# Performance work log

Hardware: AMD Instinct MI355X
Metric: run time of the kernel (lower is better)

Reference implementation:

```python
import jax, jax.numpy as jnp
import numpy as np

N = 100000
D = 128
NEG_SLOPE = 0.2


def setup_inputs() -> dict:
    key = jax.random.key(0)
    ks = jax.random.split(key, 10)
    x = jax.random.normal(ks[0], (N, D), dtype=jnp.float32)
    edge_index = jax.random.randint(ks[1], (2, 625000), 0, N, dtype=jnp.int64)
    s = 1.0 / np.sqrt(D)
    W1 = jax.random.uniform(ks[2], (D, D), jnp.float32, -s, s)
    a_src1 = jax.random.uniform(ks[3], (D,), jnp.float32, -s, s)
    a_dst1 = jax.random.uniform(ks[4], (D,), jnp.float32, -s, s)
    b1 = jnp.zeros((D,), jnp.float32)
    W2 = jax.random.uniform(ks[5], (D, D), jnp.float32, -s, s)
    a_src2 = jax.random.uniform(ks[6], (D,), jnp.float32, -s, s)
    a_dst2 = jax.random.uniform(ks[7], (D,), jnp.float32, -s, s)
    b2 = jnp.zeros((D,), jnp.float32)
    return {"x": x, "edge_index": edge_index, "W1": W1, "a_src1": a_src1,
            "a_dst1": a_dst1, "b1": b1, "W2": W2, "a_src2": a_src2,
            "a_dst2": a_dst2, "b2": b2}


def _add_self_loops(edge_index, n):
    loops = jnp.arange(n, dtype=edge_index.dtype)
    return jnp.concatenate([edge_index, jnp.stack([loops, loops])], axis=1)


def _gat_conv(x, src, dst, W, a_src, a_dst, b, n):
    # Linear transform: [N, D]
    h = x @ W
    # Per-node attention logits, gathered onto edges (heads=1)
    e = jnp.take(h @ a_src, src) + jnp.take(h @ a_dst, dst)  # [E]
    e = jax.nn.leaky_relu(e, NEG_SLOPE)
    # Scatter-softmax over destination-node segments (every node has a self loop)
    m = jax.ops.segment_max(e, dst, num_segments=n)
    w = jnp.exp(e - jnp.take(m, dst))
    z = jax.ops.segment_sum(w, dst, num_segments=n)
    alpha = w / jnp.take(z, dst)  # [E]
    # Weighted scatter-add aggregate
    msg = alpha[:, None] * jnp.take(h, src, axis=0)  # [E, D]
    out = jax.ops.segment_sum(msg, dst, num_segments=n)
    return out + b


def reference(x, edge_index, W1, a_src1, a_dst1, b1, W2, a_src2, a_dst2, b2):
    n = x.shape[0]
    ei = _add_self_loops(edge_index, n)
    src, dst = ei[0], ei[1]
    h = jax.nn.relu(_gat_conv(x, src, dst, W1, a_src1, a_dst1, b1, n))
    h = jax.nn.relu(_gat_conv(h, src, dst, W2, a_src2, a_dst2, b2, n))
    return h
```

## Files before the change

### kernel.cpp

```cpp
#include <hip/hip_runtime.h>

#define D 128
#define WS (D + 8)
#define NEG_SLOPE 0.2f
#define SLOTS 20
#define OVF_CAP 4096

using v8f16 = __attribute__((ext_vector_type(8))) _Float16;
using v2h   = __attribute__((ext_vector_type(2))) _Float16;
using f32x4 = __attribute__((ext_vector_type(4))) float;


__global__ __launch_bounds__(256) void prep_kernel(const float* __restrict__ W1,
        const float* __restrict__ W2, _Float16* __restrict__ Wt1,
        _Float16* __restrict__ Wt2, int* __restrict__ cnt,
        int* __restrict__ ovf_n, int n) {
    int t = blockIdx.x * 256 + threadIdx.x;
    if (t == 0) *ovf_n = 0;
    for (int i = t; i < n; i += 32768) cnt[i] = 0;
    int which = t >> 14;
    int idx = t & 16383;
    int k = idx & (D - 1);
    int c = idx >> 7;
    const float* W = which ? W2 : W1;
    _Float16* Wt = which ? Wt2 : Wt1;
    Wt[(size_t)c * D + k] = (_Float16)W[(size_t)k * D + c];
}


template<bool F16IN>
__device__ __forceinline__ void gemm_body(int bid, const void* __restrict__ Xv,
        const _Float16* __restrict__ Wt, const float* __restrict__ a_src,
        const float* __restrict__ a_dst, _Float16* __restrict__ H,
        float* __restrict__ hs, float* __restrict__ hd, int n,
        _Float16* wl) {
    const int lane = threadIdx.x & 63;
    const int wave = threadIdx.x >> 6;
    const int gl = lane & 15;
    const int q = lane >> 4;
    const int row0 = bid * 128 + wave * 16;

    int arow = row0 + gl;
    if (arow >= n) arow = n - 1;

    v8f16 afr[4];
    #pragma unroll
    for (int kc = 0; kc < 4; ++kc) {
        if constexpr (F16IN) {
            const _Float16* Xh = (const _Float16*)Xv;
            afr[kc] = *(const v8f16*)&Xh[(size_t)arow * D + kc * 32 + q * 8];
        } else {
            const float* p = &((const float*)Xv)[(size_t)arow * D + kc * 32 + q * 8];
            float4 x0 = *(const float4*)p;
            float4 x1 = *(const float4*)(p + 4);
            v8f16 t;
            t[0] = (_Float16)x0.x; t[1] = (_Float16)x0.y;
            t[2] = (_Float16)x0.z; t[3] = (_Float16)x0.w;
            t[4] = (_Float16)x1.x; t[5] = (_Float16)x1.y;
            t[6] = (_Float16)x1.z; t[7] = (_Float16)x1.w;
            afr[kc] = t;
        }
    }

    for (int i = threadIdx.x; i < D * D / 8; i += 512) {
        int r = i >> 4;
        int c = (i & 15) * 8;
        *(v8f16*)&wl[r * WS + c] = *(const v8f16*)&Wt[r * D + c];
    }
    __syncthreads();

    f32x4 acc[8];
    #pragma unroll
    for (int t = 0; t < 8; ++t) acc[t] = (f32x4){0.f, 0.f, 0.f, 0.f};

    #pragma unroll
    for (int kc = 0; kc < 4; ++kc) {
        #pragma unroll
        for (int t = 0; t < 8; ++t) {
            v8f16 bfr = *(const v8f16*)&wl[(t * 16 + gl) * WS + kc * 32 + q * 8];
            acc[t] = __builtin_amdgcn_mfma_f32_16x16x32_f16(afr[kc], bfr, acc[t], 0, 0, 0);
        }
    }

    float asv[8], adv[8];
    #pragma unroll
    for (int t = 0; t < 8; ++t) { asv[t] = a_src[t * 16 + gl]; adv[t] = a_dst[t * 16 + gl]; }

    #pragma unroll
    for (int r = 0; r < 4; ++r) {
        int row = row0 + q * 4 + r;
        bool ok = row < n;
        float ps = 0.f, pd = 0.f;
        #pragma unroll
        for (int t = 0; t < 8; ++t) {
            float v = acc[t][r];
            ps = fmaf(v, asv[t], ps);
            pd = fmaf(v, adv[t], pd);
            if (ok) H[(size_t)row * D + t * 16 + gl] = (_Float16)v;
        }
        #pragma unroll
        for (int dlt = 8; dlt > 0; dlt >>= 1) {
            ps += __shfl_down(ps, dlt, 16);
            pd += __shfl_down(pd, dlt, 16);
        }
        if (ok && gl == 0) { hs[row] = ps; hd[row] = pd; }
    }
}


__global__ __launch_bounds__(512) void mega1_kernel(
        const float* __restrict__ x, const _Float16* __restrict__ Wt1,
        const float* __restrict__ a_src1, const float* __restrict__ a_dst1,
        _Float16* __restrict__ h, float* __restrict__ hs, float* __restrict__ hd,
        const int* __restrict__ ei, int* __restrict__ cnt, int* __restrict__ csr,
        int* __restrict__ ovf_n, int* __restrict__ ovf,
        int gb, int e_in, int n) {
    __shared__ _Float16 wl[D * WS];
    int b = blockIdx.x;
    int rid;
    if (b < 2 * gb) {
        if ((b & 1) == 0) {
            gemm_body<false>(b >> 1, x, Wt1, a_src1, a_dst1, h, hs, hd, n, wl);
            return;
        }
        rid = b >> 1;
    } else {
        rid = b - gb;
    }
    int e = rid * 512 + threadIdx.x;
    int tot = e_in + n;
    if (e >= tot) return;
    int s, d;
    if (e < e_in) { s = ei[e]; d = ei[e_in + e]; }
    else          { s = e - e_in; d = s; }
    int r = atomicAdd(&cnt[d], 1);
    if (r < SLOTS) {
        csr[d * SLOTS + r] = s;
    } else {
        int ix = atomicAdd(ovf_n, 1);
        if (ix < OVF_CAP) { ovf[2 * ix] = d; ovf[2 * ix + 1] = s; }
    }
}

__global__ __launch_bounds__(512) void gemm2_kernel(
        const _Float16* __restrict__ tb, const _Float16* __restrict__ Wt2,
        const float* __restrict__ a_src2, const float* __restrict__ a_dst2,
        _Float16* __restrict__ h, float* __restrict__ hs, float* __restrict__ hd,
        int n) {
    __shared__ _Float16 wl[D * WS];
    gemm_body<true>(blockIdx.x, tb, Wt2, a_src2, a_dst2, h, hs, hd, n, wl);
}


__device__ __forceinline__ v2h pack_lo(uint a, uint b) {
    v2h r;
    r.x = __builtin_bit_cast(_Float16, (unsigned short)(a & 0xffffu));
    r.y = __builtin_bit_cast(_Float16, (unsigned short)(b & 0xffffu));
    return r;
}
__device__ __forceinline__ v2h pack_hi(uint a, uint b) {
    v2h r;
    r.x = __builtin_bit_cast(_Float16, (unsigned short)(a >> 16));
    r.y = __builtin_bit_cast(_Float16, (unsigned short)(b >> 16));
    return r;
}
__device__ __forceinline__ float lo_f(uint a) {
    return (float)__builtin_bit_cast(_Float16, (unsigned short)(a & 0xffffu));
}
__device__ __forceinline__ float hi_f(uint a) {
    return (float)__builtin_bit_cast(_Float16, (unsigned short)(a >> 16));
}

template<bool OUT_F16>
__global__ __launch_bounds__(256) void aggregate_kernel(
        const _Float16* __restrict__ h, const float* __restrict__ hs,
        const float* __restrict__ hd, const int* __restrict__ cnt,
        const int* __restrict__ csr, const int* __restrict__ ovf_n,
        const int* __restrict__ ovf, const float* __restrict__ bias,
        float* __restrict__ outf, _Float16* __restrict__ outb, int n) {
    int node = blockIdx.x * 4 + (threadIdx.x >> 6);
    if (node >= n) return;
    int lane = threadIdx.x & 63;
    int grp = lane >> 4;
    int gl = lane & 15;
    int deg = cnt[node];
    int mind = deg < SLOTS ? deg : SLOTS;
    const int base = node * SLOTS;
    float hdn = hd[node];
    const uint* hp = (const uint*)h;

    float acc[8] = {0.f, 0.f, 0.f, 0.f, 0.f, 0.f, 0.f, 0.f};
    float z = 0.f;

    int nt = (mind + 7) >> 3;

    for (int u = 0; u < nt; ++u) {
        int i0 = u * 8 + grp * 2;
        bool a0 = i0 < mind;
        bool a1 = i0 + 1 < mind;
        int s0 = a0 ? csr[base + i0] : node;
        int s1 = a1 ? csr[base + i0 + 1] : node;
        uint4 rA = *(const uint4*)(hp + ((size_t)s0 << 6) + (gl << 2));
        uint4 rB = *(const uint4*)(hp + ((size_t)s1 << 6) + (gl << 2));
        float e0 = hs[s0] + hdn;
        e0 = e0 > 0.f ? e0 : NEG_SLOPE * e0;
        float e1 = hs[s1] + hdn;
        e1 = e1 > 0.f ? e1 : NEG_SLOPE * e1;
        float w0 = a0 ? __expf(e0) : 0.f;
        float w1 = a1 ? __expf(e1) : 0.f;
        z += w0 + w1;
#if __has_builtin(__builtin_amdgcn_fdot2)
        v2h wp; wp.x = (_Float16)w0; wp.y = (_Float16)w1;
        acc[0] = __builtin_amdgcn_fdot2(pack_lo(rA.x, rB.x), wp, acc[0], false);
        acc[1] = __builtin_amdgcn_fdot2(pack_hi(rA.x, rB.x), wp, acc[1], false);
        acc[2] = __builtin_amdgcn_fdot2(pack_lo(rA.y, rB.y), wp, acc[2], false);
        acc[3] = __builtin_amdgcn_fdot2(pack_hi(rA.y, rB.y), wp, acc[3], false);
        acc[4] = __builtin_amdgcn_fdot2(pack_lo(rA.z, rB.z), wp, acc[4], false);
        acc[5] = __builtin_amdgcn_fdot2(pack_hi(rA.z, rB.z), wp, acc[5], false);
        acc[6] = __builtin_amdgcn_fdot2(pack_lo(rA.w, rB.w), wp, acc[6], false);
        acc[7] = __builtin_amdgcn_fdot2(pack_hi(rA.w, rB.w), wp, acc[7], false);
#else
        acc[0] = fmaf(w0, lo_f(rA.x), acc[0]); acc[1] = fmaf(w0, hi_f(rA.x), acc[1]);
        acc[2] = fmaf(w0, lo_f(rA.y), acc[2]); acc[3] = fmaf(w0, hi_f(rA.y), acc[3]);
        acc[4] = fmaf(w0, lo_f(rA.z), acc[4]); acc[5] = fmaf(w0, hi_f(rA.z), acc[5]);
        acc[6] = fmaf(w0, lo_f(rA.w), acc[6]); acc[7] = fmaf(w0, hi_f(rA.w), acc[7]);
        acc[0] = fmaf(w1, lo_f(rB.x), acc[0]); acc[1] = fmaf(w1, hi_f(rB.x), acc[1]);
        acc[2] = fmaf(w1, lo_f(rB.y), acc[2]); acc[3] = fmaf(w1, hi_f(rB.y), acc[3]);
        acc[4] = fmaf(w1, lo_f(rB.z), acc[4]); acc[5] = fmaf(w1, hi_f(rB.z), acc[5]);
        acc[6] = fmaf(w1, lo_f(rB.w), acc[6]); acc[7] = fmaf(w1, hi_f(rB.w), acc[7]);
#endif
    }

    if (deg > SLOTS) {
        int m = *ovf_n;
        if (m > OVF_CAP) m = OVF_CAP;
        for (int i = 0; i < m; ++i) {
            int od = ovf[2 * i];
            if (od == node) {
                int os = ovf[2 * i + 1];
                float e = hs[os] + hdn;
                e = e > 0.f ? e : NEG_SLOPE * e;
                float wv = __expf(e);
                if (grp == 0) {
                    uint4 rr = *(const uint4*)(hp + ((size_t)os << 6) + (gl << 2));
                    acc[0] = fmaf(wv, lo_f(rr.x), acc[0]); acc[1] = fmaf(wv, hi_f(rr.x), acc[1]);
                    acc[2] = fmaf(wv, lo_f(rr.y), acc[2]); acc[3] = fmaf(wv, hi_f(rr.y), acc[3]);
                    acc[4] = fmaf(wv, lo_f(rr.z), acc[4]); acc[5] = fmaf(wv, hi_f(rr.z), acc[5]);
                    acc[6] = fmaf(wv, lo_f(rr.w), acc[6]); acc[7] = fmaf(wv, hi_f(rr.w), acc[7]);
                    z += wv;
                }
            }
        }
    }

    #pragma unroll
    for (int dlt = 32; dlt >= 16; dlt >>= 1) {
        #pragma unroll
        for (int k = 0; k < 8; ++k) acc[k] += __shfl_down(acc[k], dlt, 64);
        z += __shfl_down(z, dlt, 64);
    }
    if (lane < 16) {
        float inv = 1.0f / z;
        float4 b0 = *(const float4*)&bias[lane * 8];
        float4 b1 = *(const float4*)&bias[lane * 8 + 4];
        float o[8];
        o[0] = acc[0] * inv + b0.x; o[1] = acc[1] * inv + b0.y;
        o[2] = acc[2] * inv + b0.z; o[3] = acc[3] * inv + b0.w;
        o[4] = acc[4] * inv + b1.x; o[5] = acc[5] * inv + b1.y;
        o[6] = acc[6] * inv + b1.z; o[7] = acc[7] * inv + b1.w;
        #pragma unroll
        for (int k = 0; k < 8; ++k) o[k] = o[k] > 0.f ? o[k] : 0.f;
        if constexpr (OUT_F16) {
            alignas(16) _Float16 ob[8];
            #pragma unroll
            for (int k = 0; k < 8; ++k) ob[k] = (_Float16)o[k];
            *(uint4*)&outb[(size_t)node * D + lane * 8] = *(const uint4*)ob;
        } else {
            float* op = outf + (size_t)node * D + lane * 8;
            *(float4*)op = make_float4(o[0], o[1], o[2], o[3]);
            *(float4*)(op + 4) = make_float4(o[4], o[5], o[6], o[7]);
        }
    }
}


extern "C" void kernel_launch(void* const* d_in, const int* in_sizes, int n_in,
                              void* d_out, int out_size, void* d_ws, size_t ws_size,
                              hipStream_t stream) {
    const float* x      = (const float*)d_in[0];
    const int*   ei     = (const int*)d_in[1];
    const float* W1     = (const float*)d_in[2];
    const float* a_src1 = (const float*)d_in[3];
    const float* a_dst1 = (const float*)d_in[4];
    const float* b1     = (const float*)d_in[5];
    const float* W2     = (const float*)d_in[6];
    const float* a_src2 = (const float*)d_in[7];
    const float* a_dst2 = (const float*)d_in[8];
    const float* b2     = (const float*)d_in[9];

    int n    = in_sizes[0] / D;
    int e_in = in_sizes[1] / 2;
    int e_tot = e_in + n;

    _Float16* h   = (_Float16*)d_ws;
    _Float16* Wt1 = h + (size_t)n * D;
    _Float16* Wt2 = Wt1 + D * D;
    float* hs     = (float*)(Wt2 + D * D);
    float* hd     = hs + n;
    int*   cnt    = (int*)(hd + n);
    int*   ovf_n  = cnt + n;
    int*   ovf    = ovf_n + 1;
    int*   csr    = ovf + 2 * OVF_CAP;
    _Float16* tb  = (_Float16*)d_out;

    int eb = (e_tot + 511) / 512;
    int nb4 = (n + 3) / 4;
    int gb = (n + 127) / 128;

    prep_kernel<<<128, 256, 0, stream>>>(W1, W2, Wt1, Wt2, cnt, ovf_n, n);
    mega1_kernel<<<gb + eb, 512, 0, stream>>>(x, Wt1, a_src1, a_dst1, h, hs, hd,
                                              ei, cnt, csr, ovf_n, ovf, gb, e_in, n);
    aggregate_kernel<true><<<nb4, 256, 0, stream>>>(h, hs, hd, cnt, csr, ovf_n, ovf,
                                                    b1, nullptr, tb, n);
    gemm2_kernel<<<gb, 512, 0, stream>>>(tb, Wt2, a_src2, a_dst2, h, hs, hd, n);
    aggregate_kernel<false><<<nb4, 256, 0, stream>>>(h, hs, hd, cnt, csr, ovf_n, ovf,
                                                     b2, (float*)d_out, nullptr, n);
}
```

Before: 245.0 us.

## Preseed self-loops in prep and transpose MFMA operands for vectorized H stores

```diff
diff --git a/kernel.cpp b/kernel.cpp
--- a/kernel.cpp
+++ b/kernel.cpp
@@ -13,11 +13,11 @@
 
 __global__ __launch_bounds__(256) void prep_kernel(const float* __restrict__ W1,
         const float* __restrict__ W2, _Float16* __restrict__ Wt1,
-        _Float16* __restrict__ Wt2, int* __restrict__ cnt,
+        _Float16* __restrict__ Wt2, int* __restrict__ cnt, int* __restrict__ csr,
         int* __restrict__ ovf_n, int n) {
     int t = blockIdx.x * 256 + threadIdx.x;
     if (t == 0) *ovf_n = 0;
-    for (int i = t; i < n; i += 32768) cnt[i] = 0;
+    for (int i = t; i < n; i += 32768) { cnt[i] = 1; csr[i * SLOTS] = i; }
     int which = t >> 14;
     int idx = t & 16383;
     int k = idx & (D - 1);
@@ -41,7 +41,8 @@
     const int row0 = bid * 128 + wave * 16;
 
     int arow = row0 + gl;
-    if (arow >= n) arow = n - 1;
+    bool ok = arow < n;
+    if (!ok) arow = n - 1;
 
     v8f16 afr[4];
     #pragma unroll
@@ -78,33 +79,29 @@
         #pragma unroll
         for (int t = 0; t < 8; ++t) {
             v8f16 bfr = *(const v8f16*)&wl[(t * 16 + gl) * WS + kc * 32 + q * 8];
-            acc[t] = __builtin_amdgcn_mfma_f32_16x16x32_f16(afr[kc], bfr, acc[t], 0, 0, 0);
-        }
-    }
-
-    float asv[8], adv[8];
-    #pragma unroll
-    for (int t = 0; t < 8; ++t) { asv[t] = a_src[t * 16 + gl]; adv[t] = a_dst[t * 16 + gl]; }
-
-    #pragma unroll
-    for (int r = 0; r < 4; ++r) {
-        int row = row0 + q * 4 + r;
-        bool ok = row < n;
-        float ps = 0.f, pd = 0.f;
-        #pragma unroll
-        for (int t = 0; t < 8; ++t) {
-            float v = acc[t][r];
-            ps = fmaf(v, asv[t], ps);
-            pd = fmaf(v, adv[t], pd);
-            if (ok) H[(size_t)row * D + t * 16 + gl] = (_Float16)v;
-        }
-        #pragma unroll
-        for (int dlt = 8; dlt > 0; dlt >>= 1) {
-            ps += __shfl_down(ps, dlt, 16);
-            pd += __shfl_down(pd, dlt, 16);
-        }
-        if (ok && gl == 0) { hs[row] = ps; hd[row] = pd; }
-    }
+            acc[t] = __builtin_amdgcn_mfma_f32_16x16x32_f16(bfr, afr[kc], acc[t], 0, 0, 0);
+        }
+    }
+
+    float ps = 0.f, pd = 0.f;
+    #pragma unroll
+    for (int t = 0; t < 8; ++t) {
+        float4 as4 = *(const float4*)&a_src[t * 16 + q * 4];
+        float4 ad4 = *(const float4*)&a_dst[t * 16 + q * 4];
+        ps = fmaf(acc[t][0], as4.x, ps); pd = fmaf(acc[t][0], ad4.x, pd);
+        ps = fmaf(acc[t][1], as4.y, ps); pd = fmaf(acc[t][1], ad4.y, pd);
+        ps = fmaf(acc[t][2], as4.z, ps); pd = fmaf(acc[t][2], ad4.z, pd);
+        ps = fmaf(acc[t][3], as4.w, ps); pd = fmaf(acc[t][3], ad4.w, pd);
+        if (ok) {
+            alignas(8) _Float16 hb[4];
+            hb[0] = (_Float16)acc[t][0]; hb[1] = (_Float16)acc[t][1];
+            hb[2] = (_Float16)acc[t][2]; hb[3] = (_Float16)acc[t][3];
+            *(uint2*)&H[(size_t)arow * D + t * 16 + q * 4] = *(const uint2*)hb;
+        }
+    }
+    ps += __shfl_down(ps, 32, 64); pd += __shfl_down(pd, 32, 64);
+    ps += __shfl_down(ps, 16, 64); pd += __shfl_down(pd, 16, 64);
+    if (lane < 16 && row0 + lane < n) { hs[row0 + lane] = ps; hd[row0 + lane] = pd; }
 }
 
 
@@ -128,11 +125,9 @@
         rid = b - gb;
     }
     int e = rid * 512 + threadIdx.x;
-    int tot = e_in + n;
-    if (e >= tot) return;
-    int s, d;
-    if (e < e_in) { s = ei[e]; d = ei[e_in + e]; }
-    else          { s = e - e_in; d = s; }
+    if (e >= e_in) return;
+    int s = ei[e];
+    int d = ei[e_in + e];
     int r = atomicAdd(&cnt[d], 1);
     if (r < SLOTS) {
         csr[d * SLOTS + r] = s;
@@ -300,7 +295,6 @@
 
     int n    = in_sizes[0] / D;
     int e_in = in_sizes[1] / 2;
-    int e_tot = e_in + n;
 
     _Float16* h   = (_Float16*)d_ws;
     _Float16* Wt1 = h + (size_t)n * D;
@@ -313,11 +307,11 @@
     int*   csr    = ovf + 2 * OVF_CAP;
     _Float16* tb  = (_Float16*)d_out;
 
-    int eb = (e_tot + 511) / 512;
+    int eb = (e_in + 511) / 512;
     int nb4 = (n + 3) / 4;
     int gb = (n + 127) / 128;
 
-    prep_kernel<<<128, 256, 0, stream>>>(W1, W2, Wt1, Wt2, cnt, ovf_n, n);
+    prep_kernel<<<128, 256, 0, stream>>>(W1, W2, Wt1, Wt2, cnt, csr, ovf_n, n);
     mega1_kernel<<<gb + eb, 512, 0, stream>>>(x, Wt1, a_src1, a_dst1, h, hs, hd,
                                               ei, cnt, csr, ovf_n, ovf, gb, e_in, n);
     aggregate_kernel<true><<<nb4, 256, 0, stream>>>(h, hs, hd, cnt, csr, ovf_n, ovf,
```

Result: slower. 255.7 us (+4.4%).

## Process two destination nodes per wave and prefetch first CSR tile unconditionally

Applied to the files above, without the earlier changes.

```diff
diff --git a/kernel.cpp b/kernel.cpp
--- a/kernel.cpp
+++ b/kernel.cpp
@@ -13,11 +13,15 @@
 
 __global__ __launch_bounds__(256) void prep_kernel(const float* __restrict__ W1,
         const float* __restrict__ W2, _Float16* __restrict__ Wt1,
-        _Float16* __restrict__ Wt2, int* __restrict__ cnt,
+        _Float16* __restrict__ Wt2, int* __restrict__ cnt, int* __restrict__ csr,
         int* __restrict__ ovf_n, int n) {
     int t = blockIdx.x * 256 + threadIdx.x;
     if (t == 0) *ovf_n = 0;
-    for (int i = t; i < n; i += 32768) cnt[i] = 0;
+    for (int i = t; i < n; i += 32768) {
+        cnt[i] = 0;
+        #pragma unroll
+        for (int j = 0; j < 8; ++j) csr[i * SLOTS + j] = i;
+    }
     int which = t >> 14;
     int idx = t & 16383;
     int k = idx & (D - 1);
@@ -171,6 +175,30 @@
     return (float)__builtin_bit_cast(_Float16, (unsigned short)(a >> 16));
 }
 
+__device__ __forceinline__ void acc_pair(float* acc, const uint4& rA,
+        const uint4& rB, float w0, float w1) {
+#if __has_builtin(__builtin_amdgcn_fdot2)
+    v2h wp; wp.x = (_Float16)w0; wp.y = (_Float16)w1;
+    acc[0] = __builtin_amdgcn_fdot2(pack_lo(rA.x, rB.x), wp, acc[0], false);
+    acc[1] = __builtin_amdgcn_fdot2(pack_hi(rA.x, rB.x), wp, acc[1], false);
+    acc[2] = __builtin_amdgcn_fdot2(pack_lo(rA.y, rB.y), wp, acc[2], false);
+    acc[3] = __builtin_amdgcn_fdot2(pack_hi(rA.y, rB.y), wp, acc[3], false);
+    acc[4] = __builtin_amdgcn_fdot2(pack_lo(rA.z, rB.z), wp, acc[4], false);
+    acc[5] = __builtin_amdgcn_fdot2(pack_hi(rA.z, rB.z), wp, acc[5], false);
+    acc[6] = __builtin_amdgcn_fdot2(pack_lo(rA.w, rB.w), wp, acc[6], false);
+    acc[7] = __builtin_amdgcn_fdot2(pack_hi(rA.w, rB.w), wp, acc[7], false);
+#else
+    acc[0] = fmaf(w0, lo_f(rA.x), acc[0]); acc[1] = fmaf(w0, hi_f(rA.x), acc[1]);
+    acc[2] = fmaf(w0, lo_f(rA.y), acc[2]); acc[3] = fmaf(w0, hi_f(rA.y), acc[3]);
+    acc[4] = fmaf(w0, lo_f(rA.z), acc[4]); acc[5] = fmaf(w0, hi_f(rA.z), acc[5]);
+    acc[6] = fmaf(w0, lo_f(rA.w), acc[6]); acc[7] = fmaf(w0, hi_f(rA.w), acc[7]);
+    acc[0] = fmaf(w1, lo_f(rB.x), acc[0]); acc[1] = fmaf(w1, hi_f(rB.x), acc[1]);
+    acc[2] = fmaf(w1, lo_f(rB.y), acc[2]); acc[3] = fmaf(w1, hi_f(rB.y), acc[3]);
+    acc[4] = fmaf(w1, lo_f(rB.z), acc[4]); acc[5] = fmaf(w1, hi_f(rB.z), acc[5]);
+    acc[6] = fmaf(w1, lo_f(rB.w), acc[6]); acc[7] = fmaf(w1, hi_f(rB.w), acc[7]);
+#endif
+}
+
 template<bool OUT_F16>
 __global__ __launch_bounds__(256) void aggregate_kernel(
         const _Float16* __restrict__ h, const float* __restrict__ hs,
@@ -178,76 +206,115 @@
         const int* __restrict__ csr, const int* __restrict__ ovf_n,
         const int* __restrict__ ovf, const float* __restrict__ bias,
         float* __restrict__ outf, _Float16* __restrict__ outb, int n) {
-    int node = blockIdx.x * 4 + (threadIdx.x >> 6);
-    if (node >= n) return;
+    int nodeA = (blockIdx.x * 4 + (threadIdx.x >> 6)) * 2;
+    if (nodeA >= n) return;
+    int nodeB = nodeA + 1;
+    bool hasB = nodeB < n;
+    int nBs = hasB ? nodeB : nodeA;
     int lane = threadIdx.x & 63;
     int grp = lane >> 4;
     int gl = lane & 15;
-    int deg = cnt[node];
-    int mind = deg < SLOTS ? deg : SLOTS;
-    const int base = node * SLOTS;
-    float hdn = hd[node];
+    const int baseA = nodeA * SLOTS;
+    const int baseB = nBs * SLOTS;
     const uint* hp = (const uint*)h;
 
-    float acc[8] = {0.f, 0.f, 0.f, 0.f, 0.f, 0.f, 0.f, 0.f};
-    float z = 0.f;
-
-    int nt = (mind + 7) >> 3;
-
-    for (int u = 0; u < nt; ++u) {
-        int i0 = u * 8 + grp * 2;
-        bool a0 = i0 < mind;
-        bool a1 = i0 + 1 < mind;
-        int s0 = a0 ? csr[base + i0] : node;
-        int s1 = a1 ? csr[base + i0 + 1] : node;
-        uint4 rA = *(const uint4*)(hp + ((size_t)s0 << 6) + (gl << 2));
-        uint4 rB = *(const uint4*)(hp + ((size_t)s1 << 6) + (gl << 2));
-        float e0 = hs[s0] + hdn;
-        e0 = e0 > 0.f ? e0 : NEG_SLOPE * e0;
-        float e1 = hs[s1] + hdn;
-        e1 = e1 > 0.f ? e1 : NEG_SLOPE * e1;
-        float w0 = a0 ? __expf(e0) : 0.f;
-        float w1 = a1 ? __expf(e1) : 0.f;
-        z += w0 + w1;
-#if __has_builtin(__builtin_amdgcn_fdot2)
-        v2h wp; wp.x = (_Float16)w0; wp.y = (_Float16)w1;
-        acc[0] = __builtin_amdgcn_fdot2(pack_lo(rA.x, rB.x), wp, acc[0], false);
-        acc[1] = __builtin_amdgcn_fdot2(pack_hi(rA.x, rB.x), wp, acc[1], false);
-        acc[2] = __builtin_amdgcn_fdot2(pack_lo(rA.y, rB.y), wp, acc[2], false);
-        acc[3] = __builtin_amdgcn_fdot2(pack_hi(rA.y, rB.y), wp, acc[3], false);
-        acc[4] = __builtin_amdgcn_fdot2(pack_lo(rA.z, rB.z), wp, acc[4], false);
-        acc[5] = __builtin_amdgcn_fdot2(pack_hi(rA.z, rB.z), wp, acc[5], false);
-        acc[6] = __builtin_amdgcn_fdot2(pack_lo(rA.w, rB.w), wp, acc[6], false);
-        acc[7] = __builtin_amdgcn_fdot2(pack_hi(rA.w, rB.w), wp, acc[7], false);
-#else
-        acc[0] = fmaf(w0, lo_f(rA.x), acc[0]); acc[1] = fmaf(w0, hi_f(rA.x), acc[1]);
-        acc[2] = fmaf(w0, lo_f(rA.y), acc[2]); acc[3] = fmaf(w0, hi_f(rA.y), acc[3]);
-        acc[4] = fmaf(w0, lo_f(rA.z), acc[4]); acc[5] = fmaf(w0, hi_f(rA.z), acc[5]);
-        acc[6] = fmaf(w0, lo_f(rA.w), acc[6]); acc[7] = fmaf(w0, hi_f(rA.w), acc[7]);
-        acc[0] = fmaf(w1, lo_f(rB.x), acc[0]); acc[1] = fmaf(w1, hi_f(rB.x), acc[1]);
-        acc[2] = fmaf(w1, lo_f(rB.y), acc[2]); acc[3] = fmaf(w1, hi_f(rB.y), acc[3]);
-        acc[4] = fmaf(w1, lo_f(rB.z), acc[4]); acc[5] = fmaf(w1, hi_f(rB.z), acc[5]);
-        acc[6] = fmaf(w1, lo_f(rB.w), acc[6]); acc[7] = fmaf(w1, hi_f(rB.w), acc[7]);
-#endif
-    }
-
-    if (deg > SLOTS) {
+    int degA = cnt[nodeA];
+    int degB = cnt[nBs];
+    float hdA = hd[nodeA];
+    float hdB = hd[nBs];
+    int jb = grp * 2;
+    int cA0 = csr[baseA + jb];
+    int cA1 = csr[baseA + jb + 1];
+    int cB0 = csr[baseB + jb];
+    int cB1 = csr[baseB + jb + 1];
+    int sA0 = ((uint)cA0 < (uint)n) ? cA0 : nodeA;
+    int sA1 = ((uint)cA1 < (uint)n) ? cA1 : nodeA;
+    int sB0 = ((uint)cB0 < (uint)n) ? cB0 : nBs;
+    int sB1 = ((uint)cB1 < (uint)n) ? cB1 : nBs;
+    uint4 rA0 = *(const uint4*)(hp + ((size_t)sA0 << 6) + (gl << 2));
+    uint4 rA1 = *(const uint4*)(hp + ((size_t)sA1 << 6) + (gl << 2));
+    uint4 rB0 = *(const uint4*)(hp + ((size_t)sB0 << 6) + (gl << 2));
+    uint4 rB1 = *(const uint4*)(hp + ((size_t)sB1 << 6) + (gl << 2));
+    float eA0 = hs[sA0] + hdA;
+    float eA1 = hs[sA1] + hdA;
+    float eB0 = hs[sB0] + hdB;
+    float eB1 = hs[sB1] + hdB;
+
+    float accA[8] = {0.f, 0.f, 0.f, 0.f, 0.f, 0.f, 0.f, 0.f};
+    float accB[8] = {0.f, 0.f, 0.f, 0.f, 0.f, 0.f, 0.f, 0.f};
+    float zA = 0.f, zB = 0.f;
+
+    int mindA = degA < SLOTS ? degA : SLOTS;
+    int mindB = degB < SLOTS ? degB : SLOTS;
+    eA0 = eA0 > 0.f ? eA0 : NEG_SLOPE * eA0;
+    eA1 = eA1 > 0.f ? eA1 : NEG_SLOPE * eA1;
+    eB0 = eB0 > 0.f ? eB0 : NEG_SLOPE * eB0;
+    eB1 = eB1 > 0.f ? eB1 : NEG_SLOPE * eB1;
+    float wA0 = (jb < mindA) ? __expf(eA0) : 0.f;
+    float wA1 = (jb + 1 < mindA) ? __expf(eA1) : 0.f;
+    float wB0 = (jb < mindB) ? __expf(eB0) : 0.f;
+    float wB1 = (jb + 1 < mindB) ? __expf(eB1) : 0.f;
+    zA += wA0 + wA1;
+    zB += wB0 + wB1;
+    acc_pair(accA, rA0, rA1, wA0, wA1);
+    acc_pair(accB, rB0, rB1, wB0, wB1);
+
+    int ntA = (mindA + 7) >> 3;
+    for (int u = 1; u < ntA; ++u) {
+        int i0 = u * 8 + jb;
+        bool a0 = i0 < mindA;
+        bool a1 = i0 + 1 < mindA;
+        int t0 = a0 ? csr[baseA + i0] : nodeA;
+        int t1 = a1 ? csr[baseA + i0 + 1] : nodeA;
+        uint4 qA = *(const uint4*)(hp + ((size_t)t0 << 6) + (gl << 2));
+        uint4 qB = *(const uint4*)(hp + ((size_t)t1 << 6) + (gl << 2));
+        float f0 = hs[t0] + hdA;
+        f0 = f0 > 0.f ? f0 : NEG_SLOPE * f0;
+        float f1 = hs[t1] + hdA;
+        f1 = f1 > 0.f ? f1 : NEG_SLOPE * f1;
+        float v0 = a0 ? __expf(f0) : 0.f;
+        float v1 = a1 ? __expf(f1) : 0.f;
+        zA += v0 + v1;
+        acc_pair(accA, qA, qB, v0, v1);
+    }
+    int ntB = (mindB + 7) >> 3;
+    for (int u = 1; u < ntB; ++u) {
+        int i0 = u * 8 + jb;
+        bool a0 = i0 < mindB;
+        bool a1 = i0 + 1 < mindB;
+        int t0 = a0 ? csr[baseB + i0] : nBs;
+        int t1 = a1 ? csr[baseB + i0 + 1] : nBs;
+        uint4 qA = *(const uint4*)(hp + ((size_t)t0 << 6) + (gl << 2));
+        uint4 qB = *(const uint4*)(hp + ((size_t)t1 << 6) + (gl << 2));
+        float f0 = hs[t0] + hdB;
+        f0 = f0 > 0.f ? f0 : NEG_SLOPE * f0;
+        float f1 = hs[t1] + hdB;
+        f1 = f1 > 0.f ? f1 : NEG_SLOPE * f1;
+        float v0 = a0 ? __expf(f0) : 0.f;
+        float v1 = a1 ? __expf(f1) : 0.f;
+        zB += v0 + v1;
+        acc_pair(accB, qA, qB, v0, v1);
+    }
+
+    if (degA > SLOTS || degB > SLOTS) {
         int m = *ovf_n;
         if (m > OVF_CAP) m = OVF_CAP;
         for (int i = 0; i < m; ++i) {
             int od = ovf[2 * i];
-            if (od == node) {
+            if (od == nodeA || (hasB && od == nodeB)) {
+                bool isA = (od == nodeA);
                 int os = ovf[2 * i + 1];
-                float e = hs[os] + hdn;
+                float e = hs[os] + (isA ? hdA : hdB);
                 e = e > 0.f ? e : NEG_SLOPE * e;
                 float wv = __expf(e);
                 if (grp == 0) {
                     uint4 rr = *(const uint4*)(hp + ((size_t)os << 6) + (gl << 2));
-                    acc[0] = fmaf(wv, lo_f(rr.x), acc[0]); acc[1] = fmaf(wv, hi_f(rr.x), acc[1]);
-                    acc[2] = fmaf(wv, lo_f(rr.y), acc[2]); acc[3] = fmaf(wv, hi_f(rr.y), acc[3]);
-                    acc[4] = fmaf(wv, lo_f(rr.z), acc[4]); acc[5] = fmaf(wv, hi_f(rr.z), acc[5]);
-                    acc[6] = fmaf(wv, lo_f(rr.w), acc[6]); acc[7] = fmaf(wv, hi_f(rr.w), acc[7]);
-                    z += wv;
+                    float* ac = isA ? accA : accB;
+                    ac[0] = fmaf(wv, lo_f(rr.x), ac[0]); ac[1] = fmaf(wv, hi_f(rr.x), ac[1]);
+                    ac[2] = fmaf(wv, lo_f(rr.y), ac[2]); ac[3] = fmaf(wv, hi_f(rr.y), ac[3]);
+                    ac[4] = fmaf(wv, lo_f(rr.z), ac[4]); ac[5] = fmaf(wv, hi_f(rr.z), ac[5]);
+                    ac[6] = fmaf(wv, lo_f(rr.w), ac[6]); ac[7] = fmaf(wv, hi_f(rr.w), ac[7]);
+                    if (isA) zA += wv; else zB += wv;
                 }
             }
         }
@@ -256,29 +323,53 @@
     #pragma unroll
     for (int dlt = 32; dlt >= 16; dlt >>= 1) {
         #pragma unroll
-        for (int k = 0; k < 8; ++k) acc[k] += __shfl_down(acc[k], dlt, 64);
-        z += __shfl_down(z, dlt, 64);
+        for (int k = 0; k < 8; ++k) {
+            accA[k] += __shfl_down(accA[k], dlt, 64);
+            accB[k] += __shfl_down(accB[k], dlt, 64);
+        }
+        zA += __shfl_down(zA, dlt, 64);
+        zB += __shfl_down(zB, dlt, 64);
     }
     if (lane < 16) {
-        float inv = 1.0f / z;
         float4 b0 = *(const float4*)&bias[lane * 8];
         float4 b1 = *(const float4*)&bias[lane * 8 + 4];
-        float o[8];
-        o[0] = acc[0] * inv + b0.x; o[1] = acc[1] * inv + b0.y;
-        o[2] = acc[2] * inv + b0.z; o[3] = acc[3] * inv + b0.w;
-        o[4] = acc[4] * inv + b1.x; o[5] = acc[5] * inv + b1.y;
-        o[6] = acc[6] * inv + b1.z; o[7] = acc[7] * inv + b1.w;
-        #pragma unroll
-        for (int k = 0; k < 8; ++k) o[k] = o[k] > 0.f ? o[k] : 0.f;
+        float invA = 1.0f / zA;
+        float oA[8];
+        oA[0] = accA[0] * invA + b0.x; oA[1] = accA[1] * invA + b0.y;
+        oA[2] = accA[2] * invA + b0.z; oA[3] = accA[3] * invA + b0.w;
+        oA[4] = accA[4] * invA + b1.x; oA[5] = accA[5] * invA + b1.y;
+        oA[6] = accA[6] * invA + b1.z; oA[7] = accA[7] * invA + b1.w;
+        #pragma unroll
+        for (int k = 0; k < 8; ++k) oA[k] = oA[k] > 0.f ? oA[k] : 0.f;
         if constexpr (OUT_F16) {
             alignas(16) _Float16 ob[8];
             #pragma unroll
-            for (int k = 0; k < 8; ++k) ob[k] = (_Float16)o[k];
-            *(uint4*)&outb[(size_t)node * D + lane * 8] = *(const uint4*)ob;
+            for (int k = 0; k < 8; ++k) ob[k] = (_Float16)oA[k];
+            *(uint4*)&outb[(size_t)nodeA * D + lane * 8] = *(const uint4*)ob;
         } else {
-            float* op = outf + (size_t)node * D + lane * 8;
-            *(float4*)op = make_float4(o[0], o[1], o[2], o[3]);
-            *(float4*)(op + 4) = make_float4(o[4], o[5], o[6], o[7]);
+            float* op = outf + (size_t)nodeA * D + lane * 8;
+            *(float4*)op = make_float4(oA[0], oA[1], oA[2], oA[3]);
+            *(float4*)(op + 4) = make_float4(oA[4], oA[5], oA[6], oA[7]);
+        }
+        if (hasB) {
+            float invB = 1.0f / zB;
+            float oB[8];
+            oB[0] = accB[0] * invB + b0.x; oB[1] = accB[1] * invB + b0.y;
+            oB[2] = accB[2] * invB + b0.z; oB[3] = accB[3] * invB + b0.w;
+            oB[4] = accB[4] * invB + b1.x; oB[5] = accB[5] * invB + b1.y;
+            oB[6] = accB[6] * invB + b1.z; oB[7] = accB[7] * invB + b1.w;
+            #pragma unroll
+            for (int k = 0; k < 8; ++k) oB[k] = oB[k] > 0.f ? oB[k] : 0.f;
+            if constexpr (OUT_F16) {
+                alignas(16) _Float16 ob[8];
+                #pragma unroll
+                for (int k = 0; k < 8; ++k) ob[k] = (_Float16)oB[k];
+                *(uint4*)&outb[(size_t)nodeB * D + lane * 8] = *(const uint4*)ob;
+            } else {
+                float* op = outf + (size_t)nodeB * D + lane * 8;
+                *(float4*)op = make_float4(oB[0], oB[1], oB[2], oB[3]);
+                *(float4*)(op + 4) = make_float4(oB[4], oB[5], oB[6], oB[7]);
+            }
         }
     }
 }
@@ -314,15 +405,15 @@
     _Float16* tb  = (_Float16*)d_out;
 
     int eb = (e_tot + 511) / 512;
-    int nb4 = (n + 3) / 4;
+    int nb8 = (n + 7) / 8;
     int gb = (n + 127) / 128;
 
-    prep_kernel<<<128, 256, 0, stream>>>(W1, W2, Wt1, Wt2, cnt, ovf_n, n);
+    prep_kernel<<<128, 256, 0, stream>>>(W1, W2, Wt1, Wt2, cnt, csr, ovf_n, n);
     mega1_kernel<<<gb + eb, 512, 0, stream>>>(x, Wt1, a_src1, a_dst1, h, hs, hd,
                                               ei, cnt, csr, ovf_n, ovf, gb, e_in, n);
-    aggregate_kernel<true><<<nb4, 256, 0, stream>>>(h, hs, hd, cnt, csr, ovf_n, ovf,
+    aggregate_kernel<true><<<nb8, 256, 0, stream>>>(h, hs, hd, cnt, csr, ovf_n, ovf,
                                                     b1, nullptr, tb, n);
     gemm2_kernel<<<gb, 512, 0, stream>>>(tb, Wt2, a_src2, a_dst2, h, hs, hd, n);
-    aggregate_kernel<false><<<nb4, 256, 0, stream>>>(h, hs, hd, cnt, csr, ovf_n, ovf,
+    aggregate_kernel<false><<<nb8, 256, 0, stream>>>(h, hs, hd, cnt, csr, ovf_n, ovf,
                                                      b2, (float*)d_out, nullptr, n);
 }
```

New measurement: 229.2 us. 6.4% less time.
